# Performance work log

Measured on AMD Instinct MI355X. Metric: run time of the kernel, lower is better.

Reference implementation:

```python
import jax, jax.numpy as jnp
import numpy as np
from jax import lax

N = 50000
E = 320000
IN_DIM = 128
OUT_DIM = 64
N_CHANNEL = 8
KERNEL = 3
N_REL = 500
BN_EPS = 1e-5


def setup_inputs() -> dict:
    key = jax.random.key(0)
    ks = jax.random.split(key, 10)
    inp = jax.random.normal(ks[0], (N, IN_DIM), dtype=jnp.float32)
    heads = jax.random.randint(ks[1], (E,), 0, N)
    rels = jax.random.randint(ks[2], (E,), 0, N_REL)
    tails = jax.random.randint(ks[3], (E,), 0, N)
    triple = jnp.stack([heads, rels, tails], axis=1).astype(jnp.int64)
    # parameters
    limit_W = float(np.sqrt(6.0 / (IN_DIM + OUT_DIM)))  # xavier_uniform
    W = jax.random.uniform(ks[4], (IN_DIM, OUT_DIM), minval=-limit_W, maxval=limit_W, dtype=jnp.float32)
    rel_embed = jax.random.normal(ks[5], (N_REL, OUT_DIM), dtype=jnp.float32)
    fan_in = 1 * KERNEL * KERNEL
    b = float(1.0 / np.sqrt(fan_in))
    conv_w = jax.random.uniform(ks[6], (N_CHANNEL, 1, KERNEL, KERNEL), minval=-b, maxval=b, dtype=jnp.float32)
    conv_b = jax.random.uniform(ks[7], (N_CHANNEL,), minval=-b, maxval=b, dtype=jnp.float32)
    fc_in = N_CHANNEL * (OUT_DIM - KERNEL + 1) * (3 - KERNEL + 1)
    bf = float(1.0 / np.sqrt(fc_in))
    fc_w = jax.random.uniform(ks[8], (1, fc_in), minval=-bf, maxval=bf, dtype=jnp.float32)
    bn1_gamma = jnp.ones((1,), jnp.float32)
    bn1_beta = jnp.zeros((1,), jnp.float32)
    bn2_gamma = jnp.ones((N_CHANNEL,), jnp.float32)
    bn2_beta = jnp.zeros((N_CHANNEL,), jnp.float32)
    return {"input": inp, "triple": triple, "W": W, "rel_embed": rel_embed,
            "conv_w": conv_w, "conv_b": conv_b, "fc_w": fc_w,
            "bn1_gamma": bn1_gamma, "bn1_beta": bn1_beta,
            "bn2_gamma": bn2_gamma, "bn2_beta": bn2_beta}


def _bn_eval(x, gamma, beta):
    # eval-mode BatchNorm with running_mean=0, running_var=1
    scale = gamma / jnp.sqrt(1.0 + BN_EPS)
    return x * scale.reshape(1, -1, 1, 1) + beta.reshape(1, -1, 1, 1)


def reference(input, triple, W, rel_embed, conv_w, conv_b, fc_w,
              bn1_gamma, bn1_beta, bn2_gamma, bn2_beta):
    n = input.shape[0]
    inp = input @ W                       # [N, out_dim]
    head = triple[:, 0]
    tail = triple[:, 2]
    h = inp[head]                         # [E, D]
    r = rel_embed[triple[:, 1]]           # [E, D]
    t = inp[tail]                         # [E, D]
    # energy function: [E,1,D,3] -> bn1 -> conv -> bn2 -> relu -> fc
    x = jnp.stack([h, r, t], axis=-1)[:, None, :, :]   # [E,1,D,3]
    x = _bn_eval(x, bn1_gamma, bn1_beta)
    y = lax.conv_general_dilated(x, conv_w, (1, 1), 'VALID',
                                 dimension_numbers=('NCHW', 'OIHW', 'NCHW'))
    y = y + conv_b.reshape(1, -1, 1, 1)                 # [E,C,D-2,1]
    y = jax.nn.relu(_bn_eval(y, bn2_gamma, bn2_beta))
    y = y.reshape(y.shape[0], -1)
    e = y @ fc_w[0]                                     # [E]
    e = jax.nn.leaky_relu(e, 0.01)
    # sparse softmax over rows (head) then sparse mm with input_
    m = jax.ops.segment_max(e, head, num_segments=n)
    ex = jnp.exp(e - m[head])
    denom = jax.ops.segment_sum(ex, head, num_segments=n)
    attn = ex / denom[head]
    agg = jax.ops.segment_sum(attn[:, None] * t, head, num_segments=n)
    return jax.nn.elu(agg + inp)
```

## Files before the change

kernel.cpp:

```cpp
#include <hip/hip_runtime.h>
#include <hip/hip_bf16.h>
#include <stdint.h>

#define IN_DIM   128
#define OUT_DIM  64
#define NCH      8
#define N_REL    500
#define BN_EPS   1e-5f
#define CAP      32


#define KEEP(x) asm volatile("" : "+v"(x))

__device__ __forceinline__ float dpp_shl1(float x) {
    return __int_as_float(__builtin_amdgcn_update_dpp(
        0, __float_as_int(x), 0x130, 0xf, 0xf, true));
}

__device__ __forceinline__ float sget(float x) {
    return __int_as_float(__builtin_amdgcn_readfirstlane(__float_as_int(x)));
}

__device__ __forceinline__ void fold_cw_thread(
    const float* __restrict__ conv_w, const float* __restrict__ conv_b,
    const float* __restrict__ bn1g, const float* __restrict__ bn1b,
    const float* __restrict__ bn2g, const float* __restrict__ bn2b,
    float* __restrict__ cw, int c)
{
    if (c >= NCH) return;
    float rs  = rsqrtf(1.f + BN_EPS);
    float s1  = bn1g[0] * rs;
    float be1 = bn1b[0];
    float s2  = bn2g[c] * rs;
    float k1  = s1 * s2;
    float wsum = 0.f;
    for (int d = 0; d < 3; ++d) {
        float a  = conv_w[c * 9 + d * 3 + 0];
        float b  = conv_w[c * 9 + d * 3 + 1];
        float cc = conv_w[c * 9 + d * 3 + 2];
        wsum += a + b + cc;
        cw[c * 3 + d]      = k1 * a;
        cw[24 + c * 3 + d] = k1 * b;
        cw[48 + c * 3 + d] = k1 * cc;
    }
    cw[72 + c] = (be1 * wsum + conv_b[c]) * s2 + bn2b[c];
}

__global__ __launch_bounds__(256) void k_build(
    const float* __restrict__ X, const float* __restrict__ W,
    const int* __restrict__ triple, const float* __restrict__ rel_embed,
    const float* __restrict__ conv_w, const float* __restrict__ conv_b,
    const float* __restrict__ bn1g, const float* __restrict__ bn1b,
    const float* __restrict__ bn2g, const float* __restrict__ bn2b,
    float* __restrict__ inp, int* __restrict__ cnt, unsigned* __restrict__ rtp,
    float* __restrict__ cw, float* __restrict__ Rt,
    int E, int N, int ngemm, int nbucket)
{
    __shared__ float Wl[IN_DIM * OUT_DIM];
    __shared__ float At[64 * IN_DIM];

    if ((int)blockIdx.x < ngemm) {
        const int rows0 = blockIdx.x * 64;
        const float4* W4 = (const float4*)W;
        for (int i = threadIdx.x; i < IN_DIM * OUT_DIM / 4; i += 256)
            ((float4*)Wl)[i] = W4[i];
        for (int i = threadIdx.x; i < 64 * IN_DIM / 4; i += 256) {
            int r  = i >> 5;
            int k4 = i & 31;
            int rr = rows0 + r;
            float4 v = make_float4(0.f, 0.f, 0.f, 0.f);
            if (rr < N) v = ((const float4*)X)[(unsigned)rr * (IN_DIM / 4) + k4];
            int rsw = r ^ ((k4 & 7) << 2);
            At[(k4 * 4 + 0) * 64 + rsw] = v.x;
            At[(k4 * 4 + 1) * 64 + rsw] = v.y;
            At[(k4 * 4 + 2) * 64 + rsw] = v.z;
            At[(k4 * 4 + 3) * 64 + rsw] = v.w;
        }
        __syncthreads();

        const int tx = threadIdx.x & 15;
        const int ty = threadIdx.x >> 4;
        float a00=0.f,a01=0.f,a02=0.f,a03=0.f;
        float a10=0.f,a11=0.f,a12=0.f,a13=0.f;
        float a20=0.f,a21=0.f,a22=0.f,a23=0.f;
        float a30=0.f,a31=0.f,a32=0.f,a33=0.f;

        #pragma unroll 8
        for (int k = 0; k < IN_DIM; ++k) {
            const float4 a = *(const float4*)&At[k * 64 + ((ty * 4) ^ (((k >> 2) & 7) << 2))];
            const float4 b = *(const float4*)&Wl[k * 64 + tx * 4];
            a00 = fmaf(a.x, b.x, a00); a01 = fmaf(a.x, b.y, a01);
            a02 = fmaf(a.x, b.z, a02); a03 = fmaf(a.x, b.w, a03);
            a10 = fmaf(a.y, b.x, a10); a11 = fmaf(a.y, b.y, a11);
            a12 = fmaf(a.y, b.z, a12); a13 = fmaf(a.y, b.w, a13);
            a20 = fmaf(a.z, b.x, a20); a21 = fmaf(a.z, b.y, a21);
            a22 = fmaf(a.z, b.z, a22); a23 = fmaf(a.z, b.w, a23);
            a30 = fmaf(a.w, b.x, a30); a31 = fmaf(a.w, b.y, a31);
            a32 = fmaf(a.w, b.z, a32); a33 = fmaf(a.w, b.w, a33);
        }

        {
            int rr = rows0 + ty * 4 + 0;
            if (rr < N) *(float4*)&inp[(unsigned)rr * OUT_DIM + tx * 4] = make_float4(a00, a01, a02, a03);
            rr = rows0 + ty * 4 + 1;
            if (rr < N) *(float4*)&inp[(unsigned)rr * OUT_DIM + tx * 4] = make_float4(a10, a11, a12, a13);
            rr = rows0 + ty * 4 + 2;
            if (rr < N) *(float4*)&inp[(unsigned)rr * OUT_DIM + tx * 4] = make_float4(a20, a21, a22, a23);
            rr = rows0 + ty * 4 + 3;
            if (rr < N) *(float4*)&inp[(unsigned)rr * OUT_DIM + tx * 4] = make_float4(a30, a31, a32, a33);
        }
    } else if ((int)blockIdx.x < ngemm + nbucket) {
        const int bb   = blockIdx.x - ngemm;
        const int gtid = bb * 256 + threadIdx.x;
        if (bb == 0 && threadIdx.x < NCH)
            fold_cw_thread(conv_w, conv_b, bn1g, bn1b, bn2g, bn2b, cw, threadIdx.x);
        if (gtid < E) {
            int j = gtid;
            int h = triple[3 * j], r = triple[3 * j + 1], t = triple[3 * j + 2];
            h = min(max(h, 0), N - 1);
            r = min(max(r, 0), N_REL - 1);
            t = min(max(t, 0), N - 1);
            int pos = atomicAdd(&cnt[h], 1);
            if (pos < CAP) rtp[(unsigned)h * CAP + pos] =
                ((unsigned)r << 16) | (unsigned)t;
        }
    } else {
        const int rb  = blockIdx.x - ngemm - nbucket;
        const int ln  = threadIdx.x & 63;
        const int rel = rb * 4 + (threadIdx.x >> 6);
        if (rel < N_REL) {
            float rr = rel_embed[(unsigned)rel * OUT_DIM + ln];
            float r1 = dpp_shl1(rr), r2 = dpp_shl1(r1);
            float rs = rsqrtf(1.f + BN_EPS);
            float s1 = bn1g[0] * rs;
            float q[NCH];
            #pragma unroll
            for (int c = 0; c < NCH; ++c) {
                float k1 = s1 * (bn2g[c] * rs);
                float b0 = k1 * conv_w[c * 9 + 1];
                float b1 = k1 * conv_w[c * 9 + 4];
                float b2 = k1 * conv_w[c * 9 + 7];
                q[c] = fmaf(b0, rr, fmaf(b1, r1, b2 * r2));
            }
            float4* dst = (float4*)&Rt[(unsigned)rel * (OUT_DIM * NCH) + ln * NCH];
            dst[0] = make_float4(q[0], q[1], q[2], q[3]);
            dst[1] = make_float4(q[4], q[5], q[6], q[7]);
        }
    }
}

__device__ __forceinline__ float dpp_wave_sum(float x) {
    x += __int_as_float(__builtin_amdgcn_update_dpp(0, __float_as_int(x), 0x111, 0xf, 0xf, true));
    x += __int_as_float(__builtin_amdgcn_update_dpp(0, __float_as_int(x), 0x112, 0xf, 0xf, true));
    x += __int_as_float(__builtin_amdgcn_update_dpp(0, __float_as_int(x), 0x114, 0xf, 0xf, true));
    x += __int_as_float(__builtin_amdgcn_update_dpp(0, __float_as_int(x), 0x118, 0xf, 0xf, true));
    x += __int_as_float(__builtin_amdgcn_update_dpp(0, __float_as_int(x), 0x142, 0xf, 0xf, true));
    x += __int_as_float(__builtin_amdgcn_update_dpp(0, __float_as_int(x), 0x143, 0xf, 0xf, true));
    return __int_as_float(__builtin_amdgcn_readlane(__float_as_int(x), 63));
}

__global__ __launch_bounds__(256) void k_fused_all(
    const float* __restrict__ inp, const float* __restrict__ Rt,
    const float* __restrict__ cw, const float* __restrict__ fc_w,
    const int* __restrict__ cnt, const unsigned* __restrict__ rtp,
    float* __restrict__ out, int N)
{
    const int lane   = threadIdx.x & 63;
    const int wave   = (blockIdx.x * (blockDim.x >> 6)) + (threadIdx.x >> 6);
    const int nwaves = gridDim.x * (blockDim.x >> 6);

    float cA0[NCH], cA1[NCH], cA2[NCH], cC0[NCH], cC1[NCH], cC2[NCH], k0c[NCH];
    #pragma unroll
    for (int c = 0; c < NCH; ++c) {
        cA0[c] = sget(cw[c * 3 + 0]);
        cA1[c] = sget(cw[c * 3 + 1]);
        cA2[c] = sget(cw[c * 3 + 2]);
        cC0[c] = sget(cw[48 + c * 3 + 0]);
        cC1[c] = sget(cw[48 + c * 3 + 1]);
        cC2[c] = sget(cw[48 + c * 3 + 2]);
        k0c[c] = sget(cw[72 + c]);
    }

    float fcl[NCH];
    #pragma unroll
    for (int c = 0; c < NCH; ++c) {
        fcl[c] = (lane < 62) ? fc_w[c * 62 + lane] : 0.f;
        KEEP(fcl[c]);
    }

    for (int h = wave; h < N; h += nwaves) {
        const int deg = min(cnt[h], CAP);

        float h0 = inp[(unsigned)h * OUT_DIM + lane];
        float h1 = dpp_shl1(h0);
        float h2 = dpp_shl1(h1);
        float Ht[NCH];
        #pragma unroll
        for (int c = 0; c < NCH; ++c) {
            float v = k0c[c];
            v = fmaf(cA0[c], h0, v);
            v = fmaf(cA1[c], h1, v);
            v = fmaf(cA2[c], h2, v);
            Ht[c] = v;
            KEEP(Ht[c]);
        }

        float m_run = -INFINITY, l_run = 0.f, agg = 0.f;
        int prt = 0;
        if (lane < deg) prt = (int)rtp[(unsigned)h * CAP + lane];

        if (deg > 0) {
#define LOADE(KK, Q0, Q1, TT)                                                   \
            {   int pk  = __builtin_amdgcn_readlane(prt, (KK));                 \
                int rkL = pk >> 16, tkL = pk & 0xFFFF;                          \
                const float4* qp = (const float4*)&Rt[(unsigned)rkL * (OUT_DIM * NCH) \
                                                      + (unsigned)(lane * NCH)]; \
                Q0 = qp[0]; Q1 = qp[1];                                         \
                TT = inp[(unsigned)tkL * OUT_DIM + lane]; }

#define CHB(c, QC, T0, T1, T2, AX)                                              \
                { float y = Ht[c] + (QC);                                       \
                  y = fmaf(cC0[c], (T0), y);                                    \
                  y = fmaf(cC1[c], (T1), y);                                    \
                  y = fmaf(cC2[c], (T2), y);                                    \
                  AX = fmaf(fmaxf(y, 0.f), fcl[c], AX); }

#define CH8(Q0, Q1, T0, T1, T2, X0, X1)                                         \
                CHB(0, (Q0).x, T0, T1, T2, X0) CHB(1, (Q0).y, T0, T1, T2, X1)   \
                CHB(2, (Q0).z, T0, T1, T2, X0) CHB(3, (Q0).w, T0, T1, T2, X1)   \
                CHB(4, (Q1).x, T0, T1, T2, X0) CHB(5, (Q1).y, T0, T1, T2, X1)   \
                CHB(6, (Q1).z, T0, T1, T2, X0) CHB(7, (Q1).w, T0, T1, T2, X1)

#define SMUPD(S, TT)                                                            \
            {   float ev = fmaxf((S), 0.01f * (S));                             \
                bool  up = ev > m_run;                                          \
                float d  = up ? (m_run - ev) : (ev - m_run);                    \
                float e  = __expf(d);                                           \
                float sc = up ? e : 1.f;                                        \
                float wk = up ? 1.f : e;                                        \
                agg   = fmaf(agg, sc, wk * (TT));                               \
                l_run = fmaf(l_run, sc, wk);                                    \
                m_run = fmaxf(m_run, ev); }

            float4 qa0, qa1, qb0, qb1;
            float  tta, ttb;
            LOADE(0, qa0, qa1, tta)
            LOADE(1, qb0, qb1, ttb)

            int k = 0;
            for (; k + 1 < deg; k += 2) {
                float4 nqa0, nqa1, nqb0, nqb1;
                float  nta, ntb;
                LOADE(k + 2, nqa0, nqa1, nta)
                LOADE(k + 3, nqb0, nqb1, ntb)

                float t1a = dpp_shl1(tta), t2a = dpp_shl1(t1a);
                float t1b = dpp_shl1(ttb), t2b = dpp_shl1(t1b);
                float aA0 = 0.f, aA1 = 0.f, aB0 = 0.f, aB1 = 0.f;
                CH8(qa0, qa1, tta, t1a, t2a, aA0, aA1)
                CH8(qb0, qb1, ttb, t1b, t2b, aB0, aB1)

                float sA = dpp_wave_sum(aA0 + aA1);
                float sB = dpp_wave_sum(aB0 + aB1);

                SMUPD(sA, tta)
                SMUPD(sB, ttb)

                qa0 = nqa0; qa1 = nqa1; qb0 = nqb0; qb1 = nqb1;
                tta = nta;  ttb = ntb;
            }
            if (k < deg) {
                float t1a = dpp_shl1(tta), t2a = dpp_shl1(t1a);
                float aA0 = 0.f, aA1 = 0.f;
                CH8(qa0, qa1, tta, t1a, t2a, aA0, aA1)
                float sA = dpp_wave_sum(aA0 + aA1);
                SMUPD(sA, tta)
            }
#undef SMUPD
#undef CH8
#undef CHB
#undef LOADE
        }
        float aggn = (l_run > 0.f) ? agg / l_run : 0.f;
        float x = aggn + h0;
        float y = x > 0.f ? x : (__expf(x) - 1.f);
        out[(unsigned)h * OUT_DIM + lane] = y;
    }
}

extern "C" void kernel_launch(void* const* d_in, const int* in_sizes, int n_in,
                              void* d_out, int out_size, void* d_ws, size_t ws_size,
                              hipStream_t stream)
{
    const float* input     = (const float*)d_in[0];
    const int*   triple    = (const int*)d_in[1];
    const float* W         = (const float*)d_in[2];
    const float* rel_embed = (const float*)d_in[3];
    const float* conv_w    = (const float*)d_in[4];
    const float* conv_b    = (const float*)d_in[5];
    const float* fc_w      = (const float*)d_in[6];
    const float* bn1g      = (const float*)d_in[7];
    const float* bn1b      = (const float*)d_in[8];
    const float* bn2g      = (const float*)d_in[9];
    const float* bn2b      = (const float*)d_in[10];
    float*       out       = (float*)d_out;

    const int N = in_sizes[0] / IN_DIM;
    const int E = in_sizes[1] / 3;

    auto align = [](size_t x) { return (x + 255) & ~(size_t)255; };
    char* base = (char*)d_ws;
    size_t o = 0;
    float*    inp = (float*)(base + o);    o = align(o + (size_t)N * OUT_DIM * 4);
    unsigned* rtp = (unsigned*)(base + o); o = align(o + (size_t)N * CAP * 4);
    float*    cw  = (float*)(base + o);    o = align(o + 80 * 4);
    int*      cnt = (int*)(base + o);      o = align(o + (size_t)N * 4);
    float*    Rt  = (float*)(base + o);    o = align(o + (size_t)N_REL * OUT_DIM * NCH * 4);

    hipMemsetAsync(cnt, 0, (size_t)N * 4, stream);

    const int ngemm   = (N + 63) / 64;
    const int nbucket = (E + 255) / 256;
    const int ntab    = (N_REL + 3) / 4;
    k_build<<<ngemm + nbucket + ntab, 256, 0, stream>>>(
        input, W, triple, rel_embed, conv_w, conv_b, bn1g, bn1b, bn2g, bn2b,
        inp, cnt, rtp, cw, Rt, E, N, ngemm, nbucket);

    const int nblk = 4096;
    k_fused_all<<<nblk, 256, 0, stream>>>(inp, Rt, cw, fc_w,
                                          cnt, rtp, out, N);
}
```

Baseline: 174.7 us.

## Pack per-edge channel math into packed float2 FMAs and launch one wave per node

Rewrites the per-edge 8-channel convolution/ReLU/fc inner loop to operate on float2 vectors so the compiler can emit packed FP32 instructions (v_pk_fma_f32, packed max), halving VALU instruction count for that hot section. The prefetch of the next pair of edges is moved after the compute of the current pair, changing load/compute ordering. The grid is changed from a fixed 4096 blocks to one wave per node, removing the grid-stride loop. Packed ops need operand packing moves and use more registers, which could lower occupancy; the reordered prefetch may expose load latency.

```diff
diff --git a/kernel.cpp b/kernel.cpp
--- a/kernel.cpp
+++ b/kernel.cpp
@@ -11,6 +11,9 @@
 
 
 #define KEEP(x) asm volatile("" : "+v"(x))
+
+typedef float v2f __attribute__((ext_vector_type(2)));
+__device__ __forceinline__ v2f mk2(float a, float b) { v2f r; r.x = a; r.y = b; return r; }
 
 __device__ __forceinline__ float dpp_shl1(float x) {
     return __int_as_float(__builtin_amdgcn_update_dpp(
@@ -169,16 +172,20 @@
     const int wave   = (blockIdx.x * (blockDim.x >> 6)) + (threadIdx.x >> 6);
     const int nwaves = gridDim.x * (blockDim.x >> 6);
 
-    float cA0[NCH], cA1[NCH], cA2[NCH], cC0[NCH], cC1[NCH], cC2[NCH], k0c[NCH];
+    float cA0[NCH], cA1[NCH], cA2[NCH], k0c[NCH];
+    v2f cC0p[NCH / 2], cC1p[NCH / 2], cC2p[NCH / 2];
     #pragma unroll
     for (int c = 0; c < NCH; ++c) {
         cA0[c] = sget(cw[c * 3 + 0]);
         cA1[c] = sget(cw[c * 3 + 1]);
         cA2[c] = sget(cw[c * 3 + 2]);
-        cC0[c] = sget(cw[48 + c * 3 + 0]);
-        cC1[c] = sget(cw[48 + c * 3 + 1]);
-        cC2[c] = sget(cw[48 + c * 3 + 2]);
         k0c[c] = sget(cw[72 + c]);
+    }
+    #pragma unroll
+    for (int p = 0; p < NCH / 2; ++p) {
+        cC0p[p] = mk2(sget(cw[48 + (2 * p) * 3 + 0]), sget(cw[48 + (2 * p + 1) * 3 + 0]));
+        cC1p[p] = mk2(sget(cw[48 + (2 * p) * 3 + 1]), sget(cw[48 + (2 * p + 1) * 3 + 1]));
+        cC2p[p] = mk2(sget(cw[48 + (2 * p) * 3 + 2]), sget(cw[48 + (2 * p + 1) * 3 + 2]));
     }
 
     float fcl[NCH];
@@ -187,6 +194,11 @@
         fcl[c] = (lane < 62) ? fc_w[c * 62 + lane] : 0.f;
         KEEP(fcl[c]);
     }
+    v2f fclp[NCH / 2];
+    #pragma unroll
+    for (int p = 0; p < NCH / 2; ++p) fclp[p] = mk2(fcl[2 * p], fcl[2 * p + 1]);
+
+    const v2f zero2 = mk2(0.f, 0.f);
 
     for (int h = wave; h < N; h += nwaves) {
         const int deg = min(cnt[h], CAP);
@@ -204,6 +216,9 @@
             Ht[c] = v;
             KEEP(Ht[c]);
         }
+        v2f Ht2[NCH / 2];
+        #pragma unroll
+        for (int p = 0; p < NCH / 2; ++p) Ht2[p] = mk2(Ht[2 * p], Ht[2 * p + 1]);
 
         float m_run = -INFINITY, l_run = 0.f, agg = 0.f;
         int prt = 0;
@@ -218,18 +233,22 @@
                 Q0 = qp[0]; Q1 = qp[1];                                         \
                 TT = inp[(unsigned)tkL * OUT_DIM + lane]; }
 
-#define CHB(c, QC, T0, T1, T2, AX)                                              \
-                { float y = Ht[c] + (QC);                                       \
-                  y = fmaf(cC0[c], (T0), y);                                    \
-                  y = fmaf(cC1[c], (T1), y);                                    \
-                  y = fmaf(cC2[c], (T2), y);                                    \
-                  AX = fmaf(fmaxf(y, 0.f), fcl[c], AX); }
-
-#define CH8(Q0, Q1, T0, T1, T2, X0, X1)                                         \
-                CHB(0, (Q0).x, T0, T1, T2, X0) CHB(1, (Q0).y, T0, T1, T2, X1)   \
-                CHB(2, (Q0).z, T0, T1, T2, X0) CHB(3, (Q0).w, T0, T1, T2, X1)   \
-                CHB(4, (Q1).x, T0, T1, T2, X0) CHB(5, (Q1).y, T0, T1, T2, X1)   \
-                CHB(6, (Q1).z, T0, T1, T2, X0) CHB(7, (Q1).w, T0, T1, T2, X1)
+#define CHP(p, QP, TV0, TV1, TV2, ACC)                                          \
+                { v2f y_ = Ht2[p] + (QP);                                       \
+                  y_ = __builtin_elementwise_fma(cC0p[p], TV0, y_);             \
+                  y_ = __builtin_elementwise_fma(cC1p[p], TV1, y_);             \
+                  y_ = __builtin_elementwise_fma(cC2p[p], TV2, y_);             \
+                  y_ = __builtin_elementwise_max(y_, zero2);                    \
+                  ACC = __builtin_elementwise_fma(y_, fclp[p], ACC); }
+
+#define CH8P(Q0, Q1, T0, T1, T2, ACC)                                           \
+                { v2f tv0_ = mk2((T0), (T0));                                   \
+                  v2f tv1_ = mk2((T1), (T1));                                   \
+                  v2f tv2_ = mk2((T2), (T2));                                   \
+                  CHP(0, mk2((Q0).x, (Q0).y), tv0_, tv1_, tv2_, ACC)            \
+                  CHP(1, mk2((Q0).z, (Q0).w), tv0_, tv1_, tv2_, ACC)            \
+                  CHP(2, mk2((Q1).x, (Q1).y), tv0_, tv1_, tv2_, ACC)            \
+                  CHP(3, mk2((Q1).z, (Q1).w), tv0_, tv1_, tv2_, ACC) }
 
 #define SMUPD(S, TT)                                                            \
             {   float ev = fmaxf((S), 0.01f * (S));                             \
@@ -249,19 +268,19 @@
 
             int k = 0;
             for (; k + 1 < deg; k += 2) {
+                float t1a = dpp_shl1(tta), t2a = dpp_shl1(t1a);
+                float t1b = dpp_shl1(ttb), t2b = dpp_shl1(t1b);
+                v2f accA = zero2, accB = zero2;
+                CH8P(qa0, qa1, tta, t1a, t2a, accA)
+                CH8P(qb0, qb1, ttb, t1b, t2b, accB)
+
                 float4 nqa0, nqa1, nqb0, nqb1;
                 float  nta, ntb;
                 LOADE(k + 2, nqa0, nqa1, nta)
                 LOADE(k + 3, nqb0, nqb1, ntb)
 
-                float t1a = dpp_shl1(tta), t2a = dpp_shl1(t1a);
-                float t1b = dpp_shl1(ttb), t2b = dpp_shl1(t1b);
-                float aA0 = 0.f, aA1 = 0.f, aB0 = 0.f, aB1 = 0.f;
-                CH8(qa0, qa1, tta, t1a, t2a, aA0, aA1)
-                CH8(qb0, qb1, ttb, t1b, t2b, aB0, aB1)
-
-                float sA = dpp_wave_sum(aA0 + aA1);
-                float sB = dpp_wave_sum(aB0 + aB1);
+                float sA = dpp_wave_sum(accA.x + accA.y);
+                float sB = dpp_wave_sum(accB.x + accB.y);
 
                 SMUPD(sA, tta)
                 SMUPD(sB, ttb)
@@ -271,14 +290,14 @@
             }
             if (k < deg) {
                 float t1a = dpp_shl1(tta), t2a = dpp_shl1(t1a);
-                float aA0 = 0.f, aA1 = 0.f;
-                CH8(qa0, qa1, tta, t1a, t2a, aA0, aA1)
-                float sA = dpp_wave_sum(aA0 + aA1);
+                v2f accA = zero2;
+                CH8P(qa0, qa1, tta, t1a, t2a, accA)
+                float sA = dpp_wave_sum(accA.x + accA.y);
                 SMUPD(sA, tta)
             }
 #undef SMUPD
-#undef CH8
-#undef CHB
+#undef CH8P
+#undef CHP
 #undef LOADE
         }
         float aggn = (l_run > 0.f) ? agg / l_run : 0.f;
@@ -326,7 +345,7 @@
         input, W, triple, rel_embed, conv_w, conv_b, bn1g, bn1b, bn2g, bn2b,
         inp, cnt, rtp, cw, Rt, E, N, ngemm, nbucket);
 
-    const int nblk = 4096;
+    const int nblk = (N + 3) / 4;
     k_fused_all<<<nblk, 256, 0, stream>>>(inp, Rt, cw, fc_w,
                                           cnt, rtp, out, N);
 }
```

Result: no change. 174.7 us (-0.0%).
